# Optimization experiments

Hardware: AMD Instinct MI355X
Metric: run time of the kernel (lower is better)

## Reference

```python
import jax, jax.numpy as jnp
import numpy as np

B, N, D, E, R = 4, 4096, 64, 131072, 64

def setup_inputs() -> dict:
    key = jax.random.key(0)
    k1, k2, k3, k4 = jax.random.split(key, 4)
    z = jax.random.normal(k1, (B, N, D), dtype=jnp.float32)
    pairs = jax.random.randint(k2, (E, 2), 0, N, dtype=jnp.int64)
    # Linear params (PyTorch convention: y = x @ W.T + b), init scale ~ 1/sqrt(fan_in)
    W1 = jax.random.normal(k3, (R, 4 * D), dtype=jnp.float32) / np.sqrt(4 * D)
    b1 = jnp.zeros((R,), dtype=jnp.float32)
    W2 = jax.random.normal(k4, (R, R), dtype=jnp.float32) / np.sqrt(R)
    b2 = jnp.zeros((R,), dtype=jnp.float32)
    return {"z": z, "pairs": pairs, "W1": W1, "b1": b1, "W2": W2, "b2": b2}

def reference(z, pairs, W1, b1, W2, b2):
    # gather endpoint embeddings: [B, E, D]
    zi = z[:, pairs[:, 0], :]
    zj = z[:, pairs[:, 1], :]
    # pair feature [B, E, 4D]: concat(zi, zj, zi-zj, zi*zj)
    pair = jnp.concatenate([zi, zj, zi - zj, zi * zj], axis=-1)
    # 2-layer MLP (dropout is identity at inference)
    h = jnp.einsum('bef,rf->ber', pair, W1) + b1
    h = jax.nn.relu(h)
    h = jnp.einsum('ber,sr->bes', h, W2) + b2
    return h
```

## Files before the change

kernel.cpp:

```cpp
#include <hip/hip_runtime.h>
#include <hip/hip_bf16.h>
#include <stdint.h>


typedef __attribute__((ext_vector_type(8))) __bf16 bf16x8;
typedef __attribute__((ext_vector_type(4))) __bf16 bf16x4;
typedef __attribute__((ext_vector_type(4))) float  f32x4;

#define E_TOT 131072
#define N_TOK 4096
#define ROWS_PER_BLOCK 512
#define NSUB 4
#define Z_ELEMS (4 * N_TOK * 64)

__global__ __launch_bounds__(256) void zcast_kernel(const float* __restrict__ z,
                                                    __bf16* __restrict__ zb)
{
    const int t = blockIdx.x * 256 + threadIdx.x;
    const float4 a = ((const float4*)z)[2 * t];
    const float4 b = ((const float4*)z)[2 * t + 1];
    bf16x8 r;
    r[0] = (__bf16)a.x; r[1] = (__bf16)a.y; r[2] = (__bf16)a.z; r[3] = (__bf16)a.w;
    r[4] = (__bf16)b.x; r[5] = (__bf16)b.y; r[6] = (__bf16)b.z; r[7] = (__bf16)b.w;
    ((bf16x8*)zb)[t] = r;
}

__device__ __forceinline__ f32x4 mfma16(bf16x8 a, bf16x8 b, f32x4 c) {
    return __builtin_amdgcn_mfma_f32_16x16x32_bf16(a, b, c, 0, 0, 0);
}

__device__ __forceinline__ bf16x8 pk8(float4 a, float4 b) {
    bf16x8 r;
    r[0] = (__bf16)a.x; r[1] = (__bf16)a.y; r[2] = (__bf16)a.z; r[3] = (__bf16)a.w;
    r[4] = (__bf16)b.x; r[5] = (__bf16)b.y; r[6] = (__bf16)b.z; r[7] = (__bf16)b.w;
    return r;
}
__device__ __forceinline__ float4 f4add(float4 a, float4 b){ return make_float4(a.x+b.x, a.y+b.y, a.z+b.z, a.w+b.w); }
__device__ __forceinline__ float4 f4sub(float4 a, float4 b){ return make_float4(a.x-b.x, a.y-b.y, a.z-b.z, a.w-b.w); }

__device__ __forceinline__ bf16x8 bmul(bf16x8 a, bf16x8 b) {
    bf16x8 r;
#pragma unroll
    for (int t = 0; t < 8; ++t)
        r[t] = (__bf16)((float)a[t] * (float)b[t]);
    return r;
}

__global__ __launch_bounds__(512, 4) void PairRelationEncoder_62775241998442_kernel(
    const __bf16* __restrict__ zw, const int* __restrict__ pairs,
    const float* __restrict__ W1, const float* __restrict__ b1,
    const float* __restrict__ W2, const float* __restrict__ b2,
    float* __restrict__ out)
{
    const int tid  = threadIdx.x;
    const int wave = tid >> 6;
    const int lane = tid & 63;
    const int x = lane & 15;
    const int g = lane >> 4;

    const int bid = (int)(blockIdx.x & 7) * 128 + ((int)blockIdx.x >> 3);
    const int m0 = bid * ROWS_PER_BLOCK;
    const int b  = m0 >> 17;
    const int e0 = m0 & (E_TOT - 1);
    const __bf16* zb = zw + ((size_t)b * N_TOK * 64);

    int2 ijv[NSUB];
#pragma unroll
    for (int st = 0; st < NSUB; ++st)
        ijv[st] = *(const int2*)(pairs + 2 * (size_t)(e0 + (st * 8 + wave) * 16 + x));

    __shared__ __bf16 w1s[64 * 192];
    __shared__ __bf16 w2s[64 * 64];
    __shared__ __bf16 h1s[8][1024];
    __shared__ float  b1s[64];
    __shared__ float  b2s[64];
    __bf16* h1w = h1s[wave];

    {
        const int part = (tid >> 6) & 3;
        const int scol = tid & 63;
        const int c8b  = (tid >> 8) * 4;
        const int cswz = (scol & 7) << 4;
        if (part < 3) {
            const float* wr = W1 + (size_t)scol * 256;
            char* dst = (char*)w1s + scol * 384;
#pragma unroll
            for (int c = 0; c < 4; ++c) {
                const int c8 = c8b + c;
                float4 p0, p1;
                if (part == 0) {
                    float4 a0 = *(const float4*)(wr + c8*8);
                    float4 a1 = *(const float4*)(wr + c8*8 + 4);
                    float4 c0 = *(const float4*)(wr + 128 + c8*8);
                    float4 c1 = *(const float4*)(wr + 128 + c8*8 + 4);
                    p0 = f4add(a0, c0); p1 = f4add(a1, c1);
                } else if (part == 1) {
                    float4 a0 = *(const float4*)(wr + 64 + c8*8);
                    float4 a1 = *(const float4*)(wr + 64 + c8*8 + 4);
                    float4 c0 = *(const float4*)(wr + 128 + c8*8);
                    float4 c1 = *(const float4*)(wr + 128 + c8*8 + 4);
                    p0 = f4sub(a0, c0); p1 = f4sub(a1, c1);
                } else {
                    p0 = *(const float4*)(wr + 192 + c8*8);
                    p1 = *(const float4*)(wr + 192 + c8*8 + 4);
                }
                *(bf16x8*)(dst + ((part * 128 + c8 * 16) ^ cswz)) = pk8(p0, p1);
            }
        } else {
            const float* wr = W2 + (size_t)scol * 64;
            char* dst = (char*)w2s + scol * 128;
#pragma unroll
            for (int c = 0; c < 4; ++c) {
                const int c8 = c8b + c;
                float4 p0 = *(const float4*)(wr + c8*8);
                float4 p1 = *(const float4*)(wr + c8*8 + 4);
                *(bf16x8*)(dst + ((c8 * 16) ^ cswz)) = pk8(p0, p1);
            }
        }
        if (tid < 64)            b1s[tid] = b1[tid];
        else if (tid < 128)      b2s[tid - 64] = b2[tid - 64];
    }

    __syncthreads();

    const int sw = (x & 7) << 4;

#pragma unroll
    for (int st = 0; st < NSUB; ++st) {
        const __bf16* zri = zb + (size_t)ijv[st].x * 64;
        const __bf16* zrj = zb + (size_t)ijv[st].y * 64;

        f32x4 acc[4];
#pragma unroll
        for (int ct = 0; ct < 4; ++ct)
            acc[ct] = *(const f32x4*)(b1s + ct * 16 + g * 4);

#pragma unroll
        for (int h = 0; h < 2; ++h) {
            bf16x8 azf = *(const bf16x8*)(zri + h * 32 + g * 8);
            bf16x8 bzf = *(const bf16x8*)(zrj + h * 32 + g * 8);
            bf16x8 pzf = bmul(azf, bzf);
            const int kb = h * 64 + g * 16;
#pragma unroll
            for (int ct = 0; ct < 4; ++ct) {
                const int colr = ct * 16 + x;
                const int cswz = (colr & 7) << 4;
                const char* wb = (const char*)w1s + colr * 384;
                bf16x8 wzi = *(const bf16x8*)(wb + ((kb      ) ^ cswz));
                bf16x8 wzj = *(const bf16x8*)(wb + ((kb + 128) ^ cswz));
                bf16x8 wpr = *(const bf16x8*)(wb + ((kb + 256) ^ cswz));
                acc[ct] = mfma16(wzi, azf, acc[ct]);
                acc[ct] = mfma16(wzj, bzf, acc[ct]);
                acc[ct] = mfma16(wpr, pzf, acc[ct]);
            }
        }

#pragma unroll
        for (int ct = 0; ct < 4; ++ct) {
            bf16x4 p;
#pragma unroll
            for (int q = 0; q < 4; ++q)
                p[q] = (__bf16)fmaxf(acc[ct][q], 0.f);
            const int wo = (x * 128 + ct * 32 + g * 8) ^ sw;
            *(bf16x4*)((char*)h1w + wo) = p;
        }

        f32x4 o[4];
#pragma unroll
        for (int ct = 0; ct < 4; ++ct)
            o[ct] = *(const f32x4*)(b2s + ct * 16 + g * 4);

#pragma unroll
        for (int kk = 0; kk < 2; ++kk) {
            const int aoff = (x * 128 + kk * 64 + g * 16) ^ sw;
            const bf16x8 h1f = *(const bf16x8*)((const char*)h1w + aoff);
#pragma unroll
            for (int ct = 0; ct < 4; ++ct) {
                const int cols = ct * 16 + x;
                const bf16x8 w2f = *(const bf16x8*)((const char*)w2s + cols * 128
                                                    + ((kk * 64 + g * 16) ^ ((cols & 7) << 4)));
                o[ct] = mfma16(w2f, h1f, o[ct]);
            }
        }

        float* orow = out + ((size_t)(m0 + (st * 8 + wave) * 16 + x)) * 64;
#pragma unroll
        for (int ct = 0; ct < 4; ++ct)
            *(f32x4*)(orow + ct * 16 + g * 4) = o[ct];
    }
}

extern "C" void kernel_launch(void* const* d_in, const int* in_sizes, int n_in,
                              void* d_out, int out_size, void* d_ws, size_t ws_size,
                              hipStream_t stream) {
    const float* z     = (const float*)d_in[0];
    const int*   pairs = (const int*)  d_in[1];
    const float* W1    = (const float*)d_in[2];
    const float* b1    = (const float*)d_in[3];
    const float* W2    = (const float*)d_in[4];
    const float* b2    = (const float*)d_in[5];
    float* out = (float*)d_out;
    __bf16* zw = (__bf16*)d_ws;

    zcast_kernel<<<Z_ELEMS / (256 * 8), 256, 0, stream>>>(z, zw);

    const int total_rows = 4 * E_TOT;
    dim3 grid(total_rows / ROWS_PER_BLOCK);
    PairRelationEncoder_62775241998442_kernel<<<grid, 512, 0, stream>>>(
        zw, pairs, W1, b1, W2, b2, out);
}
```

Before: 53.21 us.

## Precompute bf16 weight image once in prep kernel and halve block size

Moves the per-block fold of W1 (zi+zj/zj-zi/product combination), the W2 conversion to swizzled bf16 and the bias copies into a single extra block of the z-cast prep kernel, which writes the result to workspace. Each main block then only copies a 32KB image into LDS with plain vector loads. Blocks are halved to 256 threads with 256 rows each, doubling the grid and reducing LDS use per block to raise occupancy. The trade-off is twice as many per-block weight copies in exchange for removing the fp32 arithmetic and conversions from every block.

Result: faster. 47.65 us (-10.4%).

```diff
diff --git a/kernel.cpp b/kernel.cpp
--- a/kernel.cpp
+++ b/kernel.cpp
@@ -9,25 +9,13 @@
 
 #define E_TOT 131072
 #define N_TOK 4096
-#define ROWS_PER_BLOCK 512
+#define ROWS_PER_BLOCK 256
 #define NSUB 4
 #define Z_ELEMS (4 * N_TOK * 64)
-
-__global__ __launch_bounds__(256) void zcast_kernel(const float* __restrict__ z,
-                                                    __bf16* __restrict__ zb)
-{
-    const int t = blockIdx.x * 256 + threadIdx.x;
-    const float4 a = ((const float4*)z)[2 * t];
-    const float4 b = ((const float4*)z)[2 * t + 1];
-    bf16x8 r;
-    r[0] = (__bf16)a.x; r[1] = (__bf16)a.y; r[2] = (__bf16)a.z; r[3] = (__bf16)a.w;
-    r[4] = (__bf16)b.x; r[5] = (__bf16)b.y; r[6] = (__bf16)b.z; r[7] = (__bf16)b.w;
-    ((bf16x8*)zb)[t] = r;
-}
-
-__device__ __forceinline__ f32x4 mfma16(bf16x8 a, bf16x8 b, f32x4 c) {
-    return __builtin_amdgcn_mfma_f32_16x16x32_bf16(a, b, c, 0, 0, 0);
-}
+#define WIMG_OFF (Z_ELEMS * 2)
+#define WIMG_W_BYTES 32768
+#define WIMG_B1 32768
+#define WIMG_B2 33024
 
 __device__ __forceinline__ bf16x8 pk8(float4 a, float4 b) {
     bf16x8 r;
@@ -38,6 +26,65 @@
 __device__ __forceinline__ float4 f4add(float4 a, float4 b){ return make_float4(a.x+b.x, a.y+b.y, a.z+b.z, a.w+b.w); }
 __device__ __forceinline__ float4 f4sub(float4 a, float4 b){ return make_float4(a.x-b.x, a.y-b.y, a.z-b.z, a.w-b.w); }
 
+__global__ __launch_bounds__(256) void prep_kernel(
+    const float* __restrict__ z, const float* __restrict__ W1, const float* __restrict__ b1,
+    const float* __restrict__ W2, const float* __restrict__ b2,
+    __bf16* __restrict__ zw, char* __restrict__ wimg)
+{
+    const int tid = threadIdx.x;
+    const int blk = blockIdx.x;
+    if (blk < 512) {
+        const int t = blk * 256 + tid;
+        const float4 a = ((const float4*)z)[2 * t];
+        const float4 b = ((const float4*)z)[2 * t + 1];
+        ((bf16x8*)zw)[t] = pk8(a, b);
+        return;
+    }
+    const int part = tid >> 6;
+    const int scol = tid & 63;
+    const int cswz = (scol & 7) << 4;
+    if (part < 3) {
+        const float* wr = W1 + (size_t)scol * 256;
+        char* dst = wimg + scol * 384;
+#pragma unroll
+        for (int c8 = 0; c8 < 8; ++c8) {
+            float4 p0, p1;
+            if (part == 0) {
+                float4 a0 = *(const float4*)(wr + c8*8);
+                float4 a1 = *(const float4*)(wr + c8*8 + 4);
+                float4 c0 = *(const float4*)(wr + 128 + c8*8);
+                float4 c1 = *(const float4*)(wr + 128 + c8*8 + 4);
+                p0 = f4add(a0, c0); p1 = f4add(a1, c1);
+            } else if (part == 1) {
+                float4 a0 = *(const float4*)(wr + 64 + c8*8);
+                float4 a1 = *(const float4*)(wr + 64 + c8*8 + 4);
+                float4 c0 = *(const float4*)(wr + 128 + c8*8);
+                float4 c1 = *(const float4*)(wr + 128 + c8*8 + 4);
+                p0 = f4sub(a0, c0); p1 = f4sub(a1, c1);
+            } else {
+                p0 = *(const float4*)(wr + 192 + c8*8);
+                p1 = *(const float4*)(wr + 192 + c8*8 + 4);
+            }
+            *(bf16x8*)(dst + ((part * 128 + c8 * 16) ^ cswz)) = pk8(p0, p1);
+        }
+    } else {
+        const float* wr = W2 + (size_t)scol * 64;
+        char* dst = wimg + 24576 + scol * 128;
+#pragma unroll
+        for (int c8 = 0; c8 < 8; ++c8) {
+            float4 p0 = *(const float4*)(wr + c8*8);
+            float4 p1 = *(const float4*)(wr + c8*8 + 4);
+            *(bf16x8*)(dst + ((c8 * 16) ^ cswz)) = pk8(p0, p1);
+        }
+    }
+    if (tid < 64)            *(float*)(wimg + WIMG_B1 + 4 * tid) = b1[tid];
+    else if (tid < 128)      *(float*)(wimg + WIMG_B2 + 4 * (tid - 64)) = b2[tid - 64];
+}
+
+__device__ __forceinline__ f32x4 mfma16(bf16x8 a, bf16x8 b, f32x4 c) {
+    return __builtin_amdgcn_mfma_f32_16x16x32_bf16(a, b, c, 0, 0, 0);
+}
+
 __device__ __forceinline__ bf16x8 bmul(bf16x8 a, bf16x8 b) {
     bf16x8 r;
 #pragma unroll
@@ -46,11 +93,9 @@
     return r;
 }
 
-__global__ __launch_bounds__(512, 4) void PairRelationEncoder_62775241998442_kernel(
-    const __bf16* __restrict__ zw, const int* __restrict__ pairs,
-    const float* __restrict__ W1, const float* __restrict__ b1,
-    const float* __restrict__ W2, const float* __restrict__ b2,
-    float* __restrict__ out)
+__global__ __launch_bounds__(256, 4) void PairRelationEncoder_62775241998442_kernel(
+    const __bf16* __restrict__ zw, const char* __restrict__ wimg,
+    const int* __restrict__ pairs, float* __restrict__ out)
 {
     const int tid  = threadIdx.x;
     const int wave = tid >> 6;
@@ -58,7 +103,7 @@
     const int x = lane & 15;
     const int g = lane >> 4;
 
-    const int bid = (int)(blockIdx.x & 7) * 128 + ((int)blockIdx.x >> 3);
+    const int bid = (int)(blockIdx.x & 7) * 256 + ((int)blockIdx.x >> 3);
     const int m0 = bid * ROWS_PER_BLOCK;
     const int b  = m0 >> 17;
     const int e0 = m0 & (E_TOT - 1);
@@ -67,59 +112,24 @@
     int2 ijv[NSUB];
 #pragma unroll
     for (int st = 0; st < NSUB; ++st)
-        ijv[st] = *(const int2*)(pairs + 2 * (size_t)(e0 + (st * 8 + wave) * 16 + x));
-
-    __shared__ __bf16 w1s[64 * 192];
-    __shared__ __bf16 w2s[64 * 64];
-    __shared__ __bf16 h1s[8][1024];
+        ijv[st] = *(const int2*)(pairs + 2 * (size_t)(e0 + (st * 4 + wave) * 16 + x));
+
+    __shared__ char   wall[32768];
+    __shared__ __bf16 h1s[4][1024];
     __shared__ float  b1s[64];
     __shared__ float  b2s[64];
     __bf16* h1w = h1s[wave];
-
-    {
-        const int part = (tid >> 6) & 3;
-        const int scol = tid & 63;
-        const int c8b  = (tid >> 8) * 4;
-        const int cswz = (scol & 7) << 4;
-        if (part < 3) {
-            const float* wr = W1 + (size_t)scol * 256;
-            char* dst = (char*)w1s + scol * 384;
-#pragma unroll
-            for (int c = 0; c < 4; ++c) {
-                const int c8 = c8b + c;
-                float4 p0, p1;
-                if (part == 0) {
-                    float4 a0 = *(const float4*)(wr + c8*8);
-                    float4 a1 = *(const float4*)(wr + c8*8 + 4);
-                    float4 c0 = *(const float4*)(wr + 128 + c8*8);
-                    float4 c1 = *(const float4*)(wr + 128 + c8*8 + 4);
-                    p0 = f4add(a0, c0); p1 = f4add(a1, c1);
-                } else if (part == 1) {
-                    float4 a0 = *(const float4*)(wr + 64 + c8*8);
-                    float4 a1 = *(const float4*)(wr + 64 + c8*8 + 4);
-                    float4 c0 = *(const float4*)(wr + 128 + c8*8);
-                    float4 c1 = *(const float4*)(wr + 128 + c8*8 + 4);
-                    p0 = f4sub(a0, c0); p1 = f4sub(a1, c1);
-                } else {
-                    p0 = *(const float4*)(wr + 192 + c8*8);
-                    p1 = *(const float4*)(wr + 192 + c8*8 + 4);
-                }
-                *(bf16x8*)(dst + ((part * 128 + c8 * 16) ^ cswz)) = pk8(p0, p1);
-            }
-        } else {
-            const float* wr = W2 + (size_t)scol * 64;
-            char* dst = (char*)w2s + scol * 128;
-#pragma unroll
-            for (int c = 0; c < 4; ++c) {
-                const int c8 = c8b + c;
-                float4 p0 = *(const float4*)(wr + c8*8);
-                float4 p1 = *(const float4*)(wr + c8*8 + 4);
-                *(bf16x8*)(dst + ((c8 * 16) ^ cswz)) = pk8(p0, p1);
-            }
-        }
-        if (tid < 64)            b1s[tid] = b1[tid];
-        else if (tid < 128)      b2s[tid - 64] = b2[tid - 64];
-    }
+    const char* w1b = wall;
+    const char* w2b = wall + 24576;
+
+#pragma unroll
+    for (int r = 0; r < 8; ++r) {
+        const int off = (r * 256 + tid) * 16;
+        float4 v = *(const float4*)(wimg + off);
+        *(float4*)(wall + off) = v;
+    }
+    if (tid < 64)            b1s[tid] = *(const float*)(wimg + WIMG_B1 + 4 * tid);
+    else if (tid < 128)      b2s[tid - 64] = *(const float*)(wimg + WIMG_B2 + 4 * (tid - 64));
 
     __syncthreads();
 
@@ -145,7 +155,7 @@
             for (int ct = 0; ct < 4; ++ct) {
                 const int colr = ct * 16 + x;
                 const int cswz = (colr & 7) << 4;
-                const char* wb = (const char*)w1s + colr * 384;
+                const char* wb = w1b + colr * 384;
                 bf16x8 wzi = *(const bf16x8*)(wb + ((kb      ) ^ cswz));
                 bf16x8 wzj = *(const bf16x8*)(wb + ((kb + 128) ^ cswz));
                 bf16x8 wpr = *(const bf16x8*)(wb + ((kb + 256) ^ cswz));
@@ -177,13 +187,13 @@
 #pragma unroll
             for (int ct = 0; ct < 4; ++ct) {
                 const int cols = ct * 16 + x;
-                const bf16x8 w2f = *(const bf16x8*)((const char*)w2s + cols * 128
+                const bf16x8 w2f = *(const bf16x8*)(w2b + cols * 128
                                                     + ((kk * 64 + g * 16) ^ ((cols & 7) << 4)));
                 o[ct] = mfma16(w2f, h1f, o[ct]);
             }
         }
 
-        float* orow = out + ((size_t)(m0 + (st * 8 + wave) * 16 + x)) * 64;
+        float* orow = out + ((size_t)(m0 + (st * 4 + wave) * 16 + x)) * 64;
 #pragma unroll
         for (int ct = 0; ct < 4; ++ct)
             *(f32x4*)(orow + ct * 16 + g * 4) = o[ct];
@@ -200,12 +210,13 @@
     const float* W2    = (const float*)d_in[4];
     const float* b2    = (const float*)d_in[5];
     float* out = (float*)d_out;
-    __bf16* zw = (__bf16*)d_ws;
-
-    zcast_kernel<<<Z_ELEMS / (256 * 8), 256, 0, stream>>>(z, zw);
+    __bf16* zw  = (__bf16*)d_ws;
+    char*   img = (char*)d_ws + WIMG_OFF;
+
+    prep_kernel<<<513, 256, 0, stream>>>(z, W1, b1, W2, b2, zw, img);
 
     const int total_rows = 4 * E_TOT;
     dim3 grid(total_rows / ROWS_PER_BLOCK);
-    PairRelationEncoder_62775241998442_kernel<<<grid, 512, 0, stream>>>(
-        zw, pairs, W1, b1, W2, b2, out);
-}
+    PairRelationEncoder_62775241998442_kernel<<<grid, 256, 0, stream>>>(
+        zw, img, pairs, out);
+}
```
